# Kernel tuning notes

Measured on AMD Instinct MI355X. Metric: run time of the kernel, lower is better.

Reference implementation:

```python
import jax, jax.numpy as jnp
import numpy as np

B, N, H, D, F = 32, 128, 256, 256, 512   # batch, nodes, gru hidden, latent dim, mlp hidden
SUP = 0.5                                 # ancestor_suppression_strength
EPS = 1e-6


def _gru(x, h, Wx, Wh, bx, bh):
    """torch.nn.GRUCell math; x,h: [..., H]."""
    gx = x @ Wx + bx
    gh = h @ Wh + bh
    rx, ux, nx = jnp.split(gx, 3, axis=-1)
    rh, uh, nh = jnp.split(gh, 3, axis=-1)
    r = jax.nn.sigmoid(rx + rh)
    u = jax.nn.sigmoid(ux + uh)
    n = jnp.tanh(nx + r * nh)
    return (1.0 - u) * n + u * h


def setup_inputs() -> dict:
    key = jax.random.key(0)
    ks = jax.random.split(key, 12)
    rn = lambda k, shape, fan: jax.random.normal(k, shape, jnp.float32) * (fan ** -0.5)
    return {
        "z": jax.random.normal(ks[0], (B, D), jnp.float32),
        "targets": jax.random.randint(ks[1], (B, N, N), 0, 2, jnp.int32),
        "W_init": rn(ks[2], (D, H), D),
        "b_init": jnp.zeros((H,), jnp.float32),
        "Wx": rn(ks[3], (H, 3 * H), H),
        "Wh": rn(ks[4], (H, 3 * H), H),
        "bx": jnp.zeros((3 * H,), jnp.float32),
        "bh": jnp.zeros((3 * H,), jnp.float32),
        "W1": rn(ks[5], (2 * H + D, F), 2 * H + D),
        "b1": jnp.zeros((F,), jnp.float32),
        "W2": rn(ks[6], (F, 1), F),
        "b2": jnp.zeros((1,), jnp.float32),
    }


def reference(z, targets, W_init, b_init, Wx, Wh, bx, bh, W1, b1, W2, b2):
    # teacher-forcing link targets: strictly lower-triangular (parents have smaller index)
    tgt = jnp.tril(targets.astype(jnp.float32), k=-1)  # [B,N,N]
    idx = jnp.arange(N)

    def decode_one(z1, t1):  # z1:[D], t1:[N,N]
        h0 = jnp.tanh(z1 @ W_init + b_init)                      # decoder_init: z -> node-0 state
        states0 = jnp.zeros((N, H), jnp.float32).at[0].set(h0)
        A0 = jnp.zeros((N, N), jnp.float32)                      # ancestor bitset: A[i,j]=1 iff j ancestor of i

        def step(carry, t):
            states, A, ll = carry
            m = (idx < t).astype(jnp.float32)                    # existing-node mask
            pooled = (states * m[:, None]).sum(0) / m.sum()      # mean aggregation
            h_prov = _gru(pooled, h0, Wx, Wh, bx, bh)            # provisional new-node state
            # parent logits: MLP([h_new, h_j, z]) for every existing node j
            feat = jnp.concatenate([jnp.broadcast_to(h_prov, (N, H)), states,
                                    jnp.broadcast_to(z1, (N, D))], axis=-1)   # [N, 2H+D]
            logits = (jax.nn.relu(feat @ W1 + b1) @ W2 + b2)[:, 0]            # [N]
            row = t1[t]                                          # teacher-forced parents of node t
            anc = jnp.minimum(row @ A, 1.0)                      # j already ancestor of a chosen parent
            q = jnp.clip(jax.nn.sigmoid(logits) * (1.0 - SUP * anc), EPS, 1.0 - EPS)
            ll = ll + (m * (row * jnp.log(q) + (1.0 - row) * jnp.log1p(-q))).sum()
            A = A.at[t].set(jnp.minimum(row + row @ A, 1.0))     # ancestors(t) = parents U their ancestors
            states = states.at[t].set(h_prov)
            m2 = (idx <= t).astype(jnp.float32)[:, None]
            pooled2 = (states * m2).sum(0) / m2.sum()
            upd = _gru(jnp.broadcast_to(pooled2, (N, H)), states, Wx, Wh, bx, bh)
            states = m2 * upd + (1.0 - m2) * states              # propagate info among generated nodes
            return (states, A, ll), None

        (states, A, ll), _ = jax.lax.scan(step, (states0, A0, jnp.zeros((), jnp.float32)),
                                          jnp.arange(1, N))
        return t1, ll                                            # link matrix (teacher forced), log-likelihood

    L, ll = jax.vmap(decode_one)(z, tgt)
    return L, ll
```

## Files before the change

### kernel.cpp

```cpp
#include <hip/hip_runtime.h>
#include <hip/hip_bf16.h>
#include <math.h>

#define Bz 32
#define Nn 128
#define Hh 256
#define Dd 256
#define Ff 512
#define Gg 768
#define NT 512

typedef short v8s __attribute__((ext_vector_type(8)));
typedef float f4  __attribute__((ext_vector_type(4)));
#define MFMA(a,b,c) __builtin_amdgcn_mfma_f32_16x16x32_bf16(a,b,c,0,0,0)

#define WS_H0    0
#define WS_GH0   (WS_H0 + Bz*Hh)
#define WS_ZW1   (WS_GH0 + Bz*Gg)
#define WS_GXP   (WS_ZW1 + Bz*Ff)
#define WS_LOGP  (WS_GXP + Bz*2*8*Gg)
#define WS_BAR   (WS_LOGP + Bz*2*8*Nn)
#define WS_XS    (WS_BAR + Bz*32)
#define WS_WB    (WS_XS + Bz*32768)

#define SM_SW    0
#define SM_SST   81920
#define SM_NLDS  147456
#define SM_GXF   155648
#define SM_HPF   158720
#define SM_GX2   159232
#define SM_GHT   159616
#define SM_BASE  160000
#define SM_BHS   160256
#define SM_PSN   160640
#define SM_LOGI  160768
#define SM_TGR   161280
#define SM_RBIT  161536
#define SM_ANCW  161568
#define SM_AMASK 161600
#define SMEM_SZ  163648

__device__ __forceinline__ unsigned short f2bf(float x) {
  unsigned u = __float_as_uint(x);
  u = u + 0x7fffu + ((u >> 16) & 1u);
  return (unsigned short)(u >> 16);
}
__device__ __forceinline__ unsigned pack2(float e, float o) {
  return (unsigned)f2bf(e) | ((unsigned)f2bf(o) << 16);
}
__device__ __forceinline__ unsigned pkbf(float x, float y) {
  __hip_bfloat162 h = __float22bfloat162_rn(make_float2(x, y));
  union { __hip_bfloat162 h; unsigned u; } c; c.h = h; return c.u;
}
__device__ __forceinline__ float bf2f(unsigned short s) {
  return __uint_as_float(((unsigned)s) << 16);
}
__device__ __forceinline__ float sigm(float x) { return 1.0f / (1.0f + __expf(-x)); }
__device__ __forceinline__ float tanh_fast(float x) { return 2.0f / (1.0f + __expf(-2.0f*x)) - 1.0f; }
__device__ __forceinline__ v8s u4v(uint4 q) { union { uint4 q; v8s v; } c; c.q = q; return c.v; }

__device__ __forceinline__ void ast32(unsigned* p, unsigned v) {
  __hip_atomic_store(p, v, __ATOMIC_RELAXED, __HIP_MEMORY_SCOPE_AGENT);
}
__device__ __forceinline__ unsigned ald32(const unsigned* p) {
  return __hip_atomic_load(p, __ATOMIC_RELAXED, __HIP_MEMORY_SCOPE_AGENT);
}
__device__ __forceinline__ void ast64(unsigned long long* p, unsigned long long v) {
  __hip_atomic_store(p, v, __ATOMIC_RELAXED, __HIP_MEMORY_SCOPE_AGENT);
}
__device__ __forceinline__ unsigned long long ald64(const unsigned long long* p) {
  return __hip_atomic_load(p, __ATOMIC_RELAXED, __HIP_MEMORY_SCOPE_AGENT);
}

__device__ __forceinline__ void waitflags(const unsigned* FLG, int lane, int r, unsigned tgt)
{
  const bool watch = (lane < 8) && (lane != r);
  for (;;) {
    const unsigned f = watch ? ald32(FLG + lane) : 0xFFFFFFFFu;
    if (__ballot(f >= tgt) == 0xFFFFFFFFFFFFFFFFull) break;
  }
  __atomic_signal_fence(__ATOMIC_ACQUIRE);
}

__global__ void __launch_bounds__(256) prep_init(
    const int* __restrict__ tg, const float* __restrict__ Wx,
    const float* __restrict__ Wh, const float* __restrict__ W1,
    float* __restrict__ ws, float* __restrict__ out)
{
  const int stride = gridDim.x * blockDim.x;
  const int t0 = blockIdx.x * blockDim.x + threadIdx.x;

  for (int i = t0; i < Bz*Nn*Nn; i += stride) {
    int col = i & (Nn-1), row = (i >> 7) & (Nn-1);
    out[i] = (col < row) ? (float)tg[i] : 0.0f;
  }
  for (int i = t0; i < Bz; i += stride) out[Bz*Nn*Nn + i] = 0.0f;

  unsigned* BARu = (unsigned*)(ws + WS_BAR);
  for (int i = t0; i < Bz*32; i += stride) BARu[i] = 0u;

  unsigned* Wb = (unsigned*)(ws + WS_WB);
  for (int i = t0; i < 160*2048; i += stride) {
    int jw = i & 3, l = (i >> 2) & 63, ks = (i >> 8) & 7, nt = i >> 11;
    int k = ks*32 + (l >> 4)*8 + 2*jw;
    int n16 = l & 15;
    float lo, hi;
    if (nt < 48)       { int c = nt*16 + n16;        lo = Wh[k*Gg + c];      hi = Wh[(k+1)*Gg + c]; }
    else if (nt < 80)  { int f = (nt-48)*16 + n16;   lo = W1[(Hh+k)*Ff + f]; hi = W1[(Hh+k+1)*Ff + f]; }
    else if (nt < 128) { int c = (nt-80)*16 + n16;   lo = Wx[k*Gg + c];      hi = Wx[(k+1)*Gg + c]; }
    else               { int f = (nt-128)*16 + n16;  lo = W1[k*Ff + f];      hi = W1[(k+1)*Ff + f]; }
    Wb[i] = pack2(lo, hi);
  }
}

__global__ void __launch_bounds__(256) prep_batch(
    const float* __restrict__ z, const float* __restrict__ Wi,
    const float* __restrict__ bi, const float* __restrict__ Wh,
    const float* __restrict__ bh, const float* __restrict__ W1,
    float* __restrict__ ws)
{
  const int b = blockIdx.x, tid = threadIdx.x;
  __shared__ float zs[Dd], h0s[Hh];
  zs[tid] = z[b*Dd + tid];
  __syncthreads();
  float acc = bi[tid];
  for (int d = 0; d < Dd; ++d) acc = fmaf(zs[d], Wi[d*Hh + tid], acc);
  const float h0 = tanhf(acc);
  h0s[tid] = h0;
  ws[WS_H0 + b*Hh + tid] = h0;
  __syncthreads();
  for (int g = tid; g < Gg; g += 256) {
    float a = bh[g];
    for (int h = 0; h < Hh; ++h) a = fmaf(h0s[h], Wh[h*Gg + g], a);
    ws[WS_GH0 + b*Gg + g] = a;
  }
  for (int f = tid; f < Ff; f += 256) {
    float a = 0.0f;
    for (int d = 0; d < Dd; ++d) a = fmaf(zs[d], W1[(2*Hh + d)*Ff + f], a);
    ws[WS_ZW1 + b*Ff + f] = a;
  }
}

__device__ __forceinline__ void G_mfma(const unsigned short* SST, const uint4* SW4,
    int mt0, bool do1, int lane, f4* acc)
{
  #pragma unroll
  for (int ks = 0; ks < 8; ++ks) {
    const v8s a0 = *(const v8s*)(SST + (mt0*8 + ks)*512 + lane*8);
    const v8s w0 = u4v(SW4[(0*8 + ks)*64 + lane]);
    const v8s w1 = u4v(SW4[(1*8 + ks)*64 + lane]);
    const v8s w2 = u4v(SW4[(2*8 + ks)*64 + lane]);
    const v8s w3 = u4v(SW4[(3*8 + ks)*64 + lane]);
    const v8s w4 = u4v(SW4[(4*8 + ks)*64 + lane]);
    const v8s w5 = u4v(SW4[(5*8 + ks)*64 + lane]);
    acc[0] = MFMA(a0,w0,acc[0]); acc[1] = MFMA(a0,w1,acc[1]);
    acc[2] = MFMA(a0,w2,acc[2]); acc[3] = MFMA(a0,w3,acc[3]);
    acc[4] = MFMA(a0,w4,acc[4]); acc[5] = MFMA(a0,w5,acc[5]);
    if (do1) {
      const v8s a1 = *(const v8s*)(SST + ((mt0+1)*8 + ks)*512 + lane*8);
      acc[6]  = MFMA(a1,w0,acc[6]);  acc[7]  = MFMA(a1,w1,acc[7]);
      acc[8]  = MFMA(a1,w2,acc[8]);  acc[9]  = MFMA(a1,w3,acc[9]);
      acc[10] = MFMA(a1,w4,acc[10]); acc[11] = MFMA(a1,w5,acc[11]);
    }
  }
}

__device__ __forceinline__ void G_epi(const f4* ac, int mt, int t, int r,
    int quad, int c16, int lane, const float* GX2, const float* BHS,
    const unsigned short* SST, unsigned short* NLDS, float* PSN)
{
  #pragma unroll
  for (int ct = 0; ct < 2; ++ct) {
    const int hcl = ct*16 + c16;
    const f4 cr = ac[0 + ct], cu = ac[2 + ct], cn = ac[4 + ct];
    const float gxr = GX2[hcl], gxu = GX2[32+hcl], gxn = GX2[64+hcl];
    const float bhr = BHS[hcl], bhu = BHS[32+hcl], bhn = BHS[64+hcl];
    float colsum = 0.0f;
    #pragma unroll
    for (int rg = 0; rg < 4; ++rg) {
      const int row = mt*16 + quad*4 + rg;
      if (row < t) {
        const int spi = ((hcl>>3)*16 + quad*4 + rg)*8 + (hcl & 7);
        const float old = bf2f(SST[(mt*8 + r)*512 + spi]);
        const float rv = sigm(gxr + cr[rg] + bhr);
        const float uv = sigm(gxu + cu[rg] + bhu);
        const float nv = tanh_fast(gxn + rv*(cn[rg] + bhn));
        const float ns = (1.0f-uv)*nv + uv*old;
        NLDS[mt*512 + spi] = f2bf(ns);
        colsum += ns;
      }
    }
    colsum += __shfl_down(colsum, 16);
    colsum += __shfl_down(colsum, 32);
    if (lane < 16) atomicAdd(&PSN[ct*16 + lane], colsum);
  }
}

__device__ __forceinline__ void L_mfma(const unsigned short* SST, const uint4* SW4,
    int mt0, bool do1, int lane, f4* acc)
{
  #pragma unroll
  for (int ks = 0; ks < 8; ++ks) {
    const v8s a0 = *(const v8s*)(SST + (mt0*8 + ks)*512 + lane*8);
    const v8s c0 = u4v(SW4[(6*8 + ks)*64 + lane]);
    const v8s c1 = u4v(SW4[(7*8 + ks)*64 + lane]);
    const v8s c2 = u4v(SW4[(8*8 + ks)*64 + lane]);
    const v8s c3 = u4v(SW4[(9*8 + ks)*64 + lane]);
    acc[0] = MFMA(a0,c0,acc[0]); acc[1] = MFMA(a0,c1,acc[1]);
    acc[2] = MFMA(a0,c2,acc[2]); acc[3] = MFMA(a0,c3,acc[3]);
    if (do1) {
      const v8s a1 = *(const v8s*)(SST + ((mt0+1)*8 + ks)*512 + lane*8);
      acc[4] = MFMA(a1,c0,acc[4]); acc[5] = MFMA(a1,c1,acc[5]);
      acc[6] = MFMA(a1,c2,acc[6]); acc[7] = MFMA(a1,c3,acc[7]);
    }
  }
}

__device__ __forceinline__ void L_epi(const f4* ac, int mt, int t,
    int quad, int c16, const float* BASE, const float* w2r, float* LOGI)
{
  #pragma unroll
  for (int rg = 0; rg < 4; ++rg) {
    float v = fmaxf(ac[0][rg] + BASE[c16],    0.0f)*w2r[0]
            + fmaxf(ac[1][rg] + BASE[16+c16], 0.0f)*w2r[1]
            + fmaxf(ac[2][rg] + BASE[32+c16], 0.0f)*w2r[2]
            + fmaxf(ac[3][rg] + BASE[48+c16], 0.0f)*w2r[3];
    v += __shfl_xor(v, 1); v += __shfl_xor(v, 2);
    v += __shfl_xor(v, 4); v += __shfl_xor(v, 8);
    const int row = mt*16 + quad*4 + rg;
    if (c16 == 0 && row < t) atomicAdd(&LOGI[row], v);
  }
}

__device__ __forceinline__ void ll_gen(int tg_, int r, int lane, float b2v,
    const unsigned* LOGPb, const unsigned* RBIT, const unsigned* ANCW,
    float* out_ll)
{
  const int pp = tg_ & 1;
  const int row = 16*r + (lane >> 2);
  float term = 0.0f;
  if (row < tg_) {
    const unsigned* Lp = LOGPb + pp*1024;
    const int rr = (lane & 3)*2;
    float s = __uint_as_float(ald32(Lp + rr*128 + row))
            + __uint_as_float(ald32(Lp + (rr+1)*128 + row));
    s += __shfl_xor(s, 1); s += __shfl_xor(s, 2);
    if ((lane & 3) == 0) {
      const int w = row >> 5;
      const float anc = (float)((ANCW[pp*4 + w] >> (row & 31)) & 1u);
      float q = sigm(b2v + s) * (1.0f - 0.5f*anc);
      q = fminf(fmaxf(q, 1e-6f), 1.0f - 1e-6f);
      const unsigned rb = (RBIT[pp*4 + w] >> (row & 31)) & 1u;
      term = rb ? logf(q) : log1pf(-q);
    }
  }
  #pragma unroll
  for (int off = 1; off < 64; off <<= 1) term += __shfl_xor(term, off);
  if (lane == 0) atomicAdd(out_ll, term);
}

__global__ void __launch_bounds__(NT) decoder_main(
    const int* __restrict__ tg,
    const float* __restrict__ bx, const float* __restrict__ bh,
    const float* __restrict__ b1, const float* __restrict__ W2,
    const float* __restrict__ b2,
    float* __restrict__ ws, float* __restrict__ out)
{
  const int blk = blockIdx.x;
  const int b = blk & 31, r = blk >> 5;
  const int tid = threadIdx.x;
  const int lane = tid & 63, wv = tid >> 6;
  const int c16 = lane & 15, quad = lane >> 4;

  extern __shared__ char smem[];
  uint4* SW4 = (uint4*)(smem + SM_SW);
  unsigned short* SST = (unsigned short*)(smem + SM_SST);
  unsigned long long* SST64 = (unsigned long long*)(smem + SM_SST);
  unsigned short* NLDS = (unsigned short*)(smem + SM_NLDS);
  unsigned* NLDSu = (unsigned*)(smem + SM_NLDS);
  unsigned long long* NLDS64 = (unsigned long long*)(smem + SM_NLDS);
  float* GXF  = (float*)(smem + SM_GXF);
  unsigned short* HPF = (unsigned short*)(smem + SM_HPF);
  float* GX2  = (float*)(smem + SM_GX2);
  float* GHT  = (float*)(smem + SM_GHT);
  float* BASE = (float*)(smem + SM_BASE);
  float* BHS  = (float*)(smem + SM_BHS);
  float* PSN  = (float*)(smem + SM_PSN);
  float* LOGI = (float*)(smem + SM_LOGI);
  unsigned char* TGRu = (unsigned char*)(smem + SM_TGR);
  unsigned* RBIT  = (unsigned*)(smem + SM_RBIT);
  unsigned* ANCW  = (unsigned*)(smem + SM_ANCW);
  unsigned* AMASK = (unsigned*)(smem + SM_AMASK);

  const float* __restrict__ h0g  = ws + WS_H0  + b*Hh;
  const float* __restrict__ gh0g = ws + WS_GH0 + b*Gg;
  const float* __restrict__ zW1g = ws + WS_ZW1 + b*Ff;
  unsigned* GXPb = (unsigned*)(ws + WS_GXP) + b*2*8*Gg;
  unsigned* LOGPb = (unsigned*)(ws + WS_LOGP) + b*2*8*Nn;
  unsigned* FLG = (unsigned*)(ws + WS_BAR) + b*32;
  unsigned long long* XS64b = (unsigned long long*)(ws + WS_XS) + b*16384;
  const uint4* WB4 = (const uint4*)(ws + WS_WB);
  float* out_ll = out + Bz*Nn*Nn + b;

  for (int i = tid; i < 16384; i += NT) ((unsigned*)SST)[i] = 0u;
  for (int i = tid; i < 4096; i += NT) NLDSu[i] = 0u;
  for (int i = tid; i < 5120; i += NT) {
    const int lt = i >> 9, q = i & 511;
    int gt;
    if (lt < 6) { const int gate = lt >> 1, tt = lt & 1; gt = gate*16 + 2*r + tt; }
    else        { gt = 48 + 4*r + (lt - 6); }
    SW4[lt*512 + q] = WB4[gt*512 + q];
  }
  for (int i = tid; i < Nn*4; i += NT) AMASK[i] = 0u;
  if (tid < 96) BHS[tid] = bh[(tid >> 5)*256 + 32*r + (tid & 31)];
  if (tid < 128) TGRu[128 + tid] = (unsigned char)tg[b*Nn*Nn + 1*Nn + tid];
  float w2r[4];
  #pragma unroll
  for (int ft = 0; ft < 4; ++ft) w2r[ft] = W2[64*r + ft*16 + c16];
  const float b2v = b2[0];
  float p_bx[3][4], p_gh[3][4], p_h0[4];
  #pragma unroll
  for (int k = 0; k < 4; ++k) {
    const int c = 4*lane + k;
    p_h0[k] = h0g[c];
    #pragma unroll
    for (int g3 = 0; g3 < 3; ++g3) {
      p_bx[g3][k] = bx[g3*256 + c];
      p_gh[g3][k] = gh0g[g3*256 + c];
    }
  }
  int colj[2]; float auxj[2];
  #pragma unroll
  for (int jj = 0; jj < 2; ++jj) {
    const int j = 2*wv + jj;
    colj[jj] = 0; auxj[jj] = 0.0f;
    if (j >= 6 && j < 12) {
      const int jx = j - 6, g = jx >> 1, tt = jx & 1;
      const int col = g*256 + 32*r + tt*16 + c16;
      colj[jj] = col; auxj[jj] = bx[col];
    } else if (j >= 12) {
      const int ft = j - 12, f = 64*r + ft*16 + c16;
      auxj[jj] = zW1g[f] + b1[f];
    }
  }
  __syncthreads();
  if (tid < Hh) {
    const int c = tid;
    SST[(c>>5)*512 + ((c>>3)&3)*128 + (c&7)] = f2bf(h0g[c]);
  }
  if (tid < 32) PSN[tid] = h0g[32*r + tid];
  __syncthreads();
  {
    union { unsigned u[4]; v8s v; } cv;
    const float4 a0 = *(const float4*)(PSN + quad*8);
    const float4 a1 = *(const float4*)(PSN + quad*8 + 4);
    cv.u[0] = pkbf(a0.x, a0.y); cv.u[1] = pkbf(a0.z, a0.w);
    cv.u[2] = pkbf(a1.x, a1.y); cv.u[3] = pkbf(a1.z, a1.w);
    const v8s avp = cv.v;
    unsigned* GXPw = GXPb + 1*8*Gg + r*Gg;
    #pragma unroll
    for (int k2 = 0; k2 < 6; ++k2) {
      const int nt = wv*6 + k2;
      f4 c = {0.0f,0.0f,0.0f,0.0f};
      c = MFMA(avp, u4v(WB4[(80 + nt)*512 + r*64 + lane]), c);
      if (quad == 0) ast32(GXPw + nt*16 + c16, __float_as_uint(c[0]));
    }
  }
  if (tid < 128) ast64(XS64b + r*128 + tid, SST64[r*128 + tid]);
  __builtin_amdgcn_s_waitcnt(0x0F70);
  __syncthreads();
  if (tid == 0) { __atomic_signal_fence(__ATOMIC_RELEASE); ast32(FLG + r, 1u); }

  for (int t = 1; t < Nn; ++t) {
    const int tp = t & 1;
    const float invt  = 1.0f / (float)t;
    const float invt1 = 1.0f / (float)(t + 1);
    const int Mr   = (t + 15) >> 4;
    const int Mtot = (t + 16) >> 4;
    const int mtc  = t >> 4;
    const int nG = (Mr + 1) >> 1, nL = (Mr + 1) >> 1;
    const int njobs = nG + nL;

    waitflags(FLG, lane, r, (unsigned)t);

    if (tid < 384) {
      const unsigned long long* GXPr = (const unsigned long long*)(GXPb + tp*8*Gg);
      unsigned long long g[8];
      #pragma unroll
      for (int rr = 0; rr < 8; ++rr) g[rr] = ald64(GXPr + rr*384 + tid);
      float s0 = 0.0f, s1 = 0.0f;
      #pragma unroll
      for (int rr = 0; rr < 8; ++rr) {
        s0 += __uint_as_float((unsigned)g[rr]);
        s1 += __uint_as_float((unsigned)(g[rr] >> 32));
      }
      GXF[2*tid]   = s0;
      GXF[2*tid+1] = s1;
    }
    if (tid < 448) {
      const unsigned long long* XSr = XS64b + ((t-1)&1)*8192;
      for (int i = tid; i < Mr*1024; i += 448) {
        if (((i >> 7) & 7) != r) SST64[i] = ald64(XSr + i);
      }
    }
    if (wv == 6) {
      const int v0 = TGRu[tp*128 + lane];
      const int v1 = TGRu[tp*128 + lane + 64];
      const unsigned long long bal0 = __ballot(lane < t && v0);
      const unsigned long long bal1 = __ballot((lane + 64) < t && v1);
      if (lane == 0) {
        RBIT[tp*4+0] = (unsigned)bal0; RBIT[tp*4+1] = (unsigned)(bal0 >> 32);
        RBIT[tp*4+2] = (unsigned)bal1; RBIT[tp*4+3] = (unsigned)(bal1 >> 32);
      }
      LOGI[lane] = 0.0f; LOGI[lane+64] = 0.0f;
      if (lane < 32) PSN[lane] = 0.0f;
      unsigned m0=0,m1=0,m2=0,m3=0;
      if (lane < t && v0) {
        m0 = AMASK[lane*4+0]; m1 = AMASK[lane*4+1];
        m2 = AMASK[lane*4+2]; m3 = AMASK[lane*4+3];
      }
      if (lane + 64 < t && v1) {
        m0 |= AMASK[(lane+64)*4+0]; m1 |= AMASK[(lane+64)*4+1];
        m2 |= AMASK[(lane+64)*4+2]; m3 |= AMASK[(lane+64)*4+3];
      }
      #pragma unroll
      for (int off = 1; off < 64; off <<= 1) {
        m0 |= __shfl_xor(m0, off); m1 |= __shfl_xor(m1, off);
        m2 |= __shfl_xor(m2, off); m3 |= __shfl_xor(m3, off);
      }
      if (lane == 0) {
        ANCW[tp*4+0] = m0; ANCW[tp*4+1] = m1;
        ANCW[tp*4+2] = m2; ANCW[tp*4+3] = m3;
      }
    }
    if (wv == 7 && t > 1) ll_gen(t-1, r, lane, b2v, LOGPb, RBIT, ANCW, out_ll);
    __syncthreads();

    {
      float hp[4];
      const float* gr = GXF + 4*lane;
      #pragma unroll
      for (int k = 0; k < 4; ++k) {
        const float rv = sigm(gr[k]*invt       + p_bx[0][k] + p_gh[0][k]);
        const float uv = sigm(gr[256+k]*invt   + p_bx[1][k] + p_gh[1][k]);
        const float nv = tanh_fast(gr[512+k]*invt + p_bx[2][k] + rv*p_gh[2][k]);
        hp[k] = (1.0f - uv)*nv + uv*p_h0[k];
      }
      uint2 pk;
      pk.x = pack2(hp[0], hp[1]); pk.y = pack2(hp[2], hp[3]);
      *(uint2*)(HPF + 4*lane) = pk;
      if (wv == 0 && lane < 4)
        AMASK[t*4 + lane] = RBIT[tp*4 + lane] | ANCW[tp*4 + lane];
      if (wv == 1 && (t & 15) == 0) {
        for (int q = lane; q < 256; q += 64) NLDSu[mtc*256 + q] = 0u;
      }
      v8s av[8];
      #pragma unroll
      for (int ks = 0; ks < 8; ++ks) av[ks] = *(const v8s*)(HPF + ks*32 + quad*8);
      #pragma unroll
      for (int jj = 0; jj < 2; ++jj) {
        const int j = 2*wv + jj;
        f4 c = {0.0f,0.0f,0.0f,0.0f};
        if (j < 6) {
          #pragma unroll
          for (int ks = 0; ks < 8; ++ks) c = MFMA(av[ks], u4v(SW4[(j*8 + ks)*64 + lane]), c);
          if (quad == 0) GHT[(j>>1)*32 + (j&1)*16 + c16] = c[0];
        } else if (j < 12) {
          const int jx = j - 6, g = jx >> 1, tt = jx & 1;
          const uint4* Bp = WB4 + (80 + g*16 + 2*r + tt)*512 + lane;
          #pragma unroll
          for (int ks = 0; ks < 8; ++ks) c = MFMA(av[ks], u4v(Bp[ks*64]), c);
          if (quad == 0) GX2[g*32 + tt*16 + c16] = (c[0] + GXF[colj[jj]])*invt1 + auxj[jj];
        } else {
          const int ft = j - 12;
          const uint4* Bp = WB4 + (128 + 4*r + ft)*512 + lane;
          #pragma unroll
          for (int ks = 0; ks < 8; ++ks) c = MFMA(av[ks], u4v(Bp[ks*64]), c);
          if (quad == 0) BASE[ft*16 + c16] = c[0] + auxj[jj];
        }
      }
    }
    __syncthreads();

    if (wv < njobs) {
      if (wv < nG) {
        const int mt0 = 2*wv;
        const bool do1 = (mt0 + 1 < Mr);
        f4 acc[12];
        #pragma unroll
        for (int i = 0; i < 12; ++i) acc[i] = (f4){0.0f,0.0f,0.0f,0.0f};
        G_mfma(SST, SW4, mt0, do1, lane, acc);
        G_epi(acc, mt0, t, r, quad, c16, lane, GX2, BHS, SST, NLDS, PSN);
        if (do1) G_epi(acc+6, mt0+1, t, r, quad, c16, lane, GX2, BHS, SST, NLDS, PSN);
      } else {
        const int mt0 = 2*(wv - nG);
        const bool do1 = (mt0 + 1 < Mr);
        f4 acc[8];
        #pragma unroll
        for (int i = 0; i < 8; ++i) acc[i] = (f4){0.0f,0.0f,0.0f,0.0f};
        L_mfma(SST, SW4, mt0, do1, lane, acc);
        L_epi(acc, mt0, t, quad, c16, BASE, w2r, LOGI);
        if (do1) L_epi(acc+4, mt0+1, t, quad, c16, BASE, w2r, LOGI);
      }
    }
    if (wv == 7 && lane < 32) {
      const int hcl = lane;
      const float rv = sigm(GX2[hcl]    + GHT[hcl]    + BHS[hcl]);
      const float uv = sigm(GX2[32+hcl] + GHT[32+hcl] + BHS[32+hcl]);
      const float nv = tanh_fast(GX2[64+hcl] + rv*(GHT[64+hcl] + BHS[64+hcl]));
      const float old = bf2f(HPF[32*r + hcl]);
      const float ns = (1.0f - uv)*nv + uv*old;
      const int spi = ((hcl>>3)*16 + (t & 15))*8 + (hcl & 7);
      NLDS[mtc*512 + spi] = f2bf(ns);
      atomicAdd(&PSN[hcl], ns);
    }
    __syncthreads();

    {
      union { unsigned u[4]; v8s v; } cv;
      const float4 a0 = *(const float4*)(PSN + quad*8);
      const float4 a1 = *(const float4*)(PSN + quad*8 + 4);
      cv.u[0] = pkbf(a0.x, a0.y); cv.u[1] = pkbf(a0.z, a0.w);
      cv.u[2] = pkbf(a1.x, a1.y); cv.u[3] = pkbf(a1.z, a1.w);
      const v8s avp = cv.v;
      unsigned* GXPw = GXPb + ((t+1)&1)*8*Gg + r*Gg;
      #pragma unroll
      for (int k2 = 0; k2 < 6; ++k2) {
        const int nt = wv*6 + k2;
        f4 c = {0.0f,0.0f,0.0f,0.0f};
        c = MFMA(avp, u4v(WB4[(80 + nt)*512 + r*64 + lane]), c);
        if (quad == 0) ast32(GXPw + nt*16 + c16, __float_as_uint(c[0]));
      }
    }
    {
      unsigned long long* XSw = XS64b + tp*8192;
      for (int i = tid; i < Mtot*128; i += NT) {
        const int mt = i >> 7, q = i & 127;
        const unsigned long long v = NLDS64[i];
        ast64(XSw + (mt*8 + r)*128 + q, v);
        SST64[(mt*8 + r)*128 + q] = v;
      }
    }
    if (tid < 64)
      ast64((unsigned long long*)LOGPb + tp*512 + r*64 + tid,
            ((const unsigned long long*)LOGI)[tid]);
    if (wv == 7 && t + 1 < Nn) {
      const int base = b*Nn*Nn + (t+1)*Nn;
      TGRu[((t+1)&1)*128 + lane]      = (unsigned char)tg[base + lane];
      TGRu[((t+1)&1)*128 + lane + 64] = (unsigned char)tg[base + lane + 64];
    }
    __builtin_amdgcn_s_waitcnt(0x0F70);
    __syncthreads();
    if (tid == 0) { __atomic_signal_fence(__ATOMIC_RELEASE); ast32(FLG + r, (unsigned)(t + 1)); }
  }

  if (wv == 7) {
    waitflags(FLG, lane, r, (unsigned)Nn);
    ll_gen(Nn - 1, r, lane, b2v, LOGPb, RBIT, ANCW, out_ll);
  }
}

extern "C" void kernel_launch(void* const* d_in, const int* in_sizes, int n_in,
                              void* d_out, int out_size, void* d_ws, size_t ws_size,
                              hipStream_t stream)
{
  const float* z  = (const float*)d_in[0];
  const int*   tg = (const int*)  d_in[1];
  const float* Wi = (const float*)d_in[2];
  const float* bi = (const float*)d_in[3];
  const float* Wx = (const float*)d_in[4];
  const float* Wh = (const float*)d_in[5];
  const float* bx = (const float*)d_in[6];
  const float* bh = (const float*)d_in[7];
  const float* W1 = (const float*)d_in[8];
  const float* b1 = (const float*)d_in[9];
  const float* W2 = (const float*)d_in[10];
  const float* b2 = (const float*)d_in[11];
  float* out = (float*)d_out;
  float* ws  = (float*)d_ws;

  hipFuncSetAttribute((const void*)decoder_main,
                      hipFuncAttributeMaxDynamicSharedMemorySize, SMEM_SZ);

  hipLaunchKernelGGL(prep_init, dim3(512), dim3(256), 0, stream, tg, Wx, Wh, W1, ws, out);
  hipLaunchKernelGGL(prep_batch, dim3(Bz), dim3(256), 0, stream, z, Wi, bi, Wh, bh, W1, ws);

  void* args[] = { (void*)&tg, (void*)&bx, (void*)&bh, (void*)&b1,
                   (void*)&W2, (void*)&b2, (void*)&ws, (void*)&out };
  hipLaunchCooperativeKernel((void*)decoder_main, dim3(256), dim3(NT),
                             args, SMEM_SZ, stream);
}
```

Before: 2.341 ms.

## Double block to 1024 threads, overlap MFMA phases, use counter barrier across blocks

Result: slower. 3.254 ms (+39.0%).

```diff
diff --git a/kernel.cpp b/kernel.cpp
--- a/kernel.cpp
+++ b/kernel.cpp
@@ -8,7 +8,7 @@
 #define Dd 256
 #define Ff 512
 #define Gg 768
-#define NT 512
+#define NT 1024
 
 typedef short v8s __attribute__((ext_vector_type(8)));
 typedef float f4  __attribute__((ext_vector_type(4)));
@@ -72,14 +72,17 @@
   return __hip_atomic_load(p, __ATOMIC_RELAXED, __HIP_MEMORY_SCOPE_AGENT);
 }
 
-__device__ __forceinline__ void waitflags(const unsigned* FLG, int lane, int r, unsigned tgt)
-{
-  const bool watch = (lane < 8) && (lane != r);
-  for (;;) {
-    const unsigned f = watch ? ald32(FLG + lane) : 0xFFFFFFFFu;
-    if (__ballot(f >= tgt) == 0xFFFFFFFFFFFFFFFFull) break;
-  }
-  __atomic_signal_fence(__ATOMIC_ACQUIRE);
+__device__ __forceinline__ void bbar(unsigned* cnt, unsigned& seq)
+{
+  __builtin_amdgcn_s_waitcnt(0x0F70);
+  __syncthreads();
+  seq += 8;
+  if (threadIdx.x == 0) {
+    __hip_atomic_fetch_add(cnt, 1u, __ATOMIC_RELAXED, __HIP_MEMORY_SCOPE_AGENT);
+    while (__hip_atomic_load(cnt, __ATOMIC_RELAXED, __HIP_MEMORY_SCOPE_AGENT) < seq)
+      __builtin_amdgcn_s_sleep(1);
+  }
+  __syncthreads();
 }
 
 __global__ void __launch_bounds__(256) prep_init(
@@ -269,7 +272,7 @@
   const int blk = blockIdx.x;
   const int b = blk & 31, r = blk >> 5;
   const int tid = threadIdx.x;
-  const int lane = tid & 63, wv = tid >> 6;
+  const int lane = tid & 63, w = tid >> 6;
   const int c16 = lane & 15, quad = lane >> 4;
 
   extern __shared__ char smem[];
@@ -297,7 +300,7 @@
   const float* __restrict__ zW1g = ws + WS_ZW1 + b*Ff;
   unsigned* GXPb = (unsigned*)(ws + WS_GXP) + b*2*8*Gg;
   unsigned* LOGPb = (unsigned*)(ws + WS_LOGP) + b*2*8*Nn;
-  unsigned* FLG = (unsigned*)(ws + WS_BAR) + b*32;
+  unsigned* bar = (unsigned*)(ws + WS_BAR) + b*32;
   unsigned long long* XS64b = (unsigned long long*)(ws + WS_XS) + b*16384;
   const uint4* WB4 = (const uint4*)(ws + WS_WB);
   float* out_ll = out + Bz*Nn*Nn + b;
@@ -319,30 +322,33 @@
   for (int ft = 0; ft < 4; ++ft) w2r[ft] = W2[64*r + ft*16 + c16];
   const float b2v = b2[0];
   float p_bx[3][4], p_gh[3][4], p_h0[4];
-  #pragma unroll
-  for (int k = 0; k < 4; ++k) {
-    const int c = 4*lane + k;
-    p_h0[k] = h0g[c];
+  int colj[2]; float auxj[2];
+  if (w >= 8) {
     #pragma unroll
-    for (int g3 = 0; g3 < 3; ++g3) {
-      p_bx[g3][k] = bx[g3*256 + c];
-      p_gh[g3][k] = gh0g[g3*256 + c];
-    }
-  }
-  int colj[2]; float auxj[2];
-  #pragma unroll
-  for (int jj = 0; jj < 2; ++jj) {
-    const int j = 2*wv + jj;
-    colj[jj] = 0; auxj[jj] = 0.0f;
-    if (j >= 6 && j < 12) {
-      const int jx = j - 6, g = jx >> 1, tt = jx & 1;
-      const int col = g*256 + 32*r + tt*16 + c16;
-      colj[jj] = col; auxj[jj] = bx[col];
-    } else if (j >= 12) {
-      const int ft = j - 12, f = 64*r + ft*16 + c16;
-      auxj[jj] = zW1g[f] + b1[f];
-    }
-  }
+    for (int k = 0; k < 4; ++k) {
+      const int c = 4*lane + k;
+      p_h0[k] = h0g[c];
+      #pragma unroll
+      for (int g3 = 0; g3 < 3; ++g3) {
+        p_bx[g3][k] = bx[g3*256 + c];
+        p_gh[g3][k] = gh0g[g3*256 + c];
+      }
+    }
+    #pragma unroll
+    for (int jj = 0; jj < 2; ++jj) {
+      const int j = (w - 8) + 8*jj;
+      colj[jj] = 0; auxj[jj] = 0.0f;
+      if (j >= 6 && j < 12) {
+        const int jx = j - 6, g = jx >> 1, tt = jx & 1;
+        const int col = g*256 + 32*r + tt*16 + c16;
+        colj[jj] = col; auxj[jj] = bx[col];
+      } else if (j >= 12) {
+        const int ft = j - 12, f = 64*r + ft*16 + c16;
+        auxj[jj] = zW1g[f] + b1[f];
+      }
+    }
+  }
+  unsigned bseq = 0;
   __syncthreads();
   if (tid < Hh) {
     const int c = tid;
@@ -359,17 +365,15 @@
     const v8s avp = cv.v;
     unsigned* GXPw = GXPb + 1*8*Gg + r*Gg;
     #pragma unroll
-    for (int k2 = 0; k2 < 6; ++k2) {
-      const int nt = wv*6 + k2;
+    for (int k2 = 0; k2 < 3; ++k2) {
+      const int nt = w*3 + k2;
       f4 c = {0.0f,0.0f,0.0f,0.0f};
       c = MFMA(avp, u4v(WB4[(80 + nt)*512 + r*64 + lane]), c);
       if (quad == 0) ast32(GXPw + nt*16 + c16, __float_as_uint(c[0]));
     }
   }
   if (tid < 128) ast64(XS64b + r*128 + tid, SST64[r*128 + tid]);
-  __builtin_amdgcn_s_waitcnt(0x0F70);
-  __syncthreads();
-  if (tid == 0) { __atomic_signal_fence(__ATOMIC_RELEASE); ast32(FLG + r, 1u); }
+  bbar(bar, bseq);
 
   for (int t = 1; t < Nn; ++t) {
     const int tp = t & 1;
@@ -378,12 +382,12 @@
     const int Mr   = (t + 15) >> 4;
     const int Mtot = (t + 16) >> 4;
     const int mtc  = t >> 4;
-    const int nG = (Mr + 1) >> 1, nL = (Mr + 1) >> 1;
-    const int njobs = nG + nL;
-
-    waitflags(FLG, lane, r, (unsigned)t);
-
-    if (tid < 384) {
+    const int nG = (Mr + 1) >> 1;
+    const int njobs = 2*nG;
+    const unsigned long long* XSr = XS64b + (1-tp)*8192;
+    unsigned long long* XSw = XS64b + tp*8192;
+
+    if (w < 6) {
       const unsigned long long* GXPr = (const unsigned long long*)(GXPb + tp*8*Gg);
       unsigned long long g[8];
       #pragma unroll
@@ -396,24 +400,16 @@
       }
       GXF[2*tid]   = s0;
       GXF[2*tid+1] = s1;
-    }
-    if (tid < 448) {
-      const unsigned long long* XSr = XS64b + ((t-1)&1)*8192;
-      for (int i = tid; i < Mr*1024; i += 448) {
+    } else if (w < 14) {
+      const int idx = tid - 384;
+      for (int i = idx; i < Mr*1024; i += 512) {
         if (((i >> 7) & 7) != r) SST64[i] = ald64(XSr + i);
       }
-    }
-    if (wv == 6) {
+    } else if (w == 14) {
       const int v0 = TGRu[tp*128 + lane];
-      const int v1 = TGRu[tp*128 + lane + 64];
+      const int v1 = TGRu[tp*128 + 64 + lane];
       const unsigned long long bal0 = __ballot(lane < t && v0);
       const unsigned long long bal1 = __ballot((lane + 64) < t && v1);
-      if (lane == 0) {
-        RBIT[tp*4+0] = (unsigned)bal0; RBIT[tp*4+1] = (unsigned)(bal0 >> 32);
-        RBIT[tp*4+2] = (unsigned)bal1; RBIT[tp*4+3] = (unsigned)(bal1 >> 32);
-      }
-      LOGI[lane] = 0.0f; LOGI[lane+64] = 0.0f;
-      if (lane < 32) PSN[lane] = 0.0f;
       unsigned m0=0,m1=0,m2=0,m3=0;
       if (lane < t && v0) {
         m0 = AMASK[lane*4+0]; m1 = AMASK[lane*4+1];
@@ -428,82 +424,95 @@
         m0 |= __shfl_xor(m0, off); m1 |= __shfl_xor(m1, off);
         m2 |= __shfl_xor(m2, off); m3 |= __shfl_xor(m3, off);
       }
-      if (lane == 0) {
-        ANCW[tp*4+0] = m0; ANCW[tp*4+1] = m1;
-        ANCW[tp*4+2] = m2; ANCW[tp*4+3] = m3;
-      }
-    }
-    if (wv == 7 && t > 1) ll_gen(t-1, r, lane, b2v, LOGPb, RBIT, ANCW, out_ll);
+      LOGI[lane] = 0.0f; LOGI[lane + 64] = 0.0f;
+      if (lane < 32) PSN[lane] = 0.0f;
+      if (lane < 4) {
+        const unsigned rbw = (lane == 0) ? (unsigned)bal0 :
+                             (lane == 1) ? (unsigned)(bal0 >> 32) :
+                             (lane == 2) ? (unsigned)bal1 : (unsigned)(bal1 >> 32);
+        const unsigned anw = (lane == 0) ? m0 : (lane == 1) ? m1 : (lane == 2) ? m2 : m3;
+        RBIT[tp*4 + lane] = rbw;
+        ANCW[tp*4 + lane] = anw;
+      }
+    } else {
+      if (t > 1) ll_gen(t-1, r, lane, b2v, LOGPb, RBIT, ANCW, out_ll);
+    }
     __syncthreads();
 
-    {
-      float hp[4];
-      const float* gr = GXF + 4*lane;
-      #pragma unroll
-      for (int k = 0; k < 4; ++k) {
-        const float rv = sigm(gr[k]*invt       + p_bx[0][k] + p_gh[0][k]);
-        const float uv = sigm(gr[256+k]*invt   + p_bx[1][k] + p_gh[1][k]);
-        const float nv = tanh_fast(gr[512+k]*invt + p_bx[2][k] + rv*p_gh[2][k]);
-        hp[k] = (1.0f - uv)*nv + uv*p_h0[k];
-      }
-      uint2 pk;
-      pk.x = pack2(hp[0], hp[1]); pk.y = pack2(hp[2], hp[3]);
-      *(uint2*)(HPF + 4*lane) = pk;
-      if (wv == 0 && lane < 4)
+    f4 acc[12];
+    #pragma unroll
+    for (int i = 0; i < 12; ++i) acc[i] = (f4){0.0f,0.0f,0.0f,0.0f};
+    int kindA = 0, mtA = 0; bool haveA = false, d1A = false;
+    if (w < 8) {
+      if (w < njobs) {
+        haveA = true;
+        if (w < nG) { kindA = 0; mtA = 2*w; }
+        else        { kindA = 1; mtA = 2*(w - nG); }
+        d1A = (mtA + 1 < Mr);
+        if (kindA == 0) G_mfma(SST, SW4, mtA, d1A, lane, acc);
+        else            L_mfma(SST, SW4, mtA, d1A, lane, acc);
+      }
+    } else {
+      if (w == 8 && lane < 4)
         AMASK[t*4 + lane] = RBIT[tp*4 + lane] | ANCW[tp*4 + lane];
-      if (wv == 1 && (t & 15) == 0) {
+      if (w == 9 && (t & 15) == 0) {
         for (int q = lane; q < 256; q += 64) NLDSu[mtc*256 + q] = 0u;
       }
-      v8s av[8];
-      #pragma unroll
-      for (int ks = 0; ks < 8; ++ks) av[ks] = *(const v8s*)(HPF + ks*32 + quad*8);
-      #pragma unroll
-      for (int jj = 0; jj < 2; ++jj) {
-        const int j = 2*wv + jj;
-        f4 c = {0.0f,0.0f,0.0f,0.0f};
-        if (j < 6) {
-          #pragma unroll
-          for (int ks = 0; ks < 8; ++ks) c = MFMA(av[ks], u4v(SW4[(j*8 + ks)*64 + lane]), c);
-          if (quad == 0) GHT[(j>>1)*32 + (j&1)*16 + c16] = c[0];
-        } else if (j < 12) {
-          const int jx = j - 6, g = jx >> 1, tt = jx & 1;
-          const uint4* Bp = WB4 + (80 + g*16 + 2*r + tt)*512 + lane;
-          #pragma unroll
-          for (int ks = 0; ks < 8; ++ks) c = MFMA(av[ks], u4v(Bp[ks*64]), c);
-          if (quad == 0) GX2[g*32 + tt*16 + c16] = (c[0] + GXF[colj[jj]])*invt1 + auxj[jj];
+      {
+        float hp[4];
+        #pragma unroll
+        for (int k = 0; k < 4; ++k) {
+          const int c = 4*lane + k;
+          const float rv = sigm(GXF[c]*invt       + p_bx[0][k] + p_gh[0][k]);
+          const float uv = sigm(GXF[256+c]*invt   + p_bx[1][k] + p_gh[1][k]);
+          const float nv = tanh_fast(GXF[512+c]*invt + p_bx[2][k] + rv*p_gh[2][k]);
+          hp[k] = (1.0f - uv)*nv + uv*p_h0[k];
+        }
+        uint2 pk;
+        pk.x = pack2(hp[0], hp[1]); pk.y = pack2(hp[2], hp[3]);
+        *(uint2*)(HPF + 4*lane) = pk;
+      }
+      {
+        v8s av[8];
+        #pragma unroll
+        for (int ks = 0; ks < 8; ++ks) av[ks] = *(const v8s*)(HPF + ks*32 + quad*8);
+        #pragma unroll
+        for (int jj = 0; jj < 2; ++jj) {
+          const int j = (w - 8) + 8*jj;
+          f4 c = {0.0f,0.0f,0.0f,0.0f};
+          if (j < 6) {
+            #pragma unroll
+            for (int ks = 0; ks < 8; ++ks) c = MFMA(av[ks], u4v(SW4[(j*8 + ks)*64 + lane]), c);
+            if (quad == 0) GHT[(j>>1)*32 + (j&1)*16 + c16] = c[0];
+          } else if (j < 12) {
+            const int jx = j - 6, g = jx >> 1, tt = jx & 1;
+            const uint4* Bp = WB4 + (80 + g*16 + 2*r + tt)*512 + lane;
+            #pragma unroll
+            for (int ks = 0; ks < 8; ++ks) c = MFMA(av[ks], u4v(Bp[ks*64]), c);
+            if (quad == 0) GX2[g*32 + tt*16 + c16] = (c[0] + GXF[colj[jj]])*invt1 + auxj[jj];
+          } else {
+            const int ft = j - 12;
+            const uint4* Bp = WB4 + (128 + 4*r + ft)*512 + lane;
+            #pragma unroll
+            for (int ks = 0; ks < 8; ++ks) c = MFMA(av[ks], u4v(Bp[ks*64]), c);
+            if (quad == 0) BASE[ft*16 + c16] = c[0] + auxj[jj];
+          }
+        }
+      }
+    }
+    __syncthreads();
+
+    if (w < 8) {
+      if (haveA) {
+        if (kindA == 0) {
+          G_epi(acc,     mtA,   t, r, quad, c16, lane, GX2, BHS, SST, NLDS, PSN);
+          if (d1A) G_epi(acc+6, mtA+1, t, r, quad, c16, lane, GX2, BHS, SST, NLDS, PSN);
         } else {
-          const int ft = j - 12;
-          const uint4* Bp = WB4 + (128 + 4*r + ft)*512 + lane;
-          #pragma unroll
-          for (int ks = 0; ks < 8; ++ks) c = MFMA(av[ks], u4v(Bp[ks*64]), c);
-          if (quad == 0) BASE[ft*16 + c16] = c[0] + auxj[jj];
+          L_epi(acc,     mtA,   t, quad, c16, BASE, w2r, LOGI);
+          if (d1A) L_epi(acc+4, mtA+1, t, quad, c16, BASE, w2r, LOGI);
         }
       }
-    }
-    __syncthreads();
-
-    if (wv < njobs) {
-      if (wv < nG) {
-        const int mt0 = 2*wv;
-        const bool do1 = (mt0 + 1 < Mr);
-        f4 acc[12];
-        #pragma unroll
-        for (int i = 0; i < 12; ++i) acc[i] = (f4){0.0f,0.0f,0.0f,0.0f};
-        G_mfma(SST, SW4, mt0, do1, lane, acc);
-        G_epi(acc, mt0, t, r, quad, c16, lane, GX2, BHS, SST, NLDS, PSN);
-        if (do1) G_epi(acc+6, mt0+1, t, r, quad, c16, lane, GX2, BHS, SST, NLDS, PSN);
-      } else {
-        const int mt0 = 2*(wv - nG);
-        const bool do1 = (mt0 + 1 < Mr);
-        f4 acc[8];
-        #pragma unroll
-        for (int i = 0; i < 8; ++i) acc[i] = (f4){0.0f,0.0f,0.0f,0.0f};
-        L_mfma(SST, SW4, mt0, do1, lane, acc);
-        L_epi(acc, mt0, t, quad, c16, BASE, w2r, LOGI);
-        if (do1) L_epi(acc+4, mt0+1, t, quad, c16, BASE, w2r, LOGI);
-      }
-    }
-    if (wv == 7 && lane < 32) {
+    } else if (w == 8 && lane < 32) {
       const int hcl = lane;
       const float rv = sigm(GX2[hcl]    + GHT[hcl]    + BHS[hcl]);
       const float uv = sigm(GX2[32+hcl] + GHT[32+hcl] + BHS[32+hcl]);
@@ -525,39 +534,31 @@
       const v8s avp = cv.v;
       unsigned* GXPw = GXPb + ((t+1)&1)*8*Gg + r*Gg;
       #pragma unroll
-      for (int k2 = 0; k2 < 6; ++k2) {
-        const int nt = wv*6 + k2;
+      for (int k2 = 0; k2 < 3; ++k2) {
+        const int nt = w*3 + k2;
         f4 c = {0.0f,0.0f,0.0f,0.0f};
         c = MFMA(avp, u4v(WB4[(80 + nt)*512 + r*64 + lane]), c);
         if (quad == 0) ast32(GXPw + nt*16 + c16, __float_as_uint(c[0]));
       }
     }
-    {
-      unsigned long long* XSw = XS64b + tp*8192;
-      for (int i = tid; i < Mtot*128; i += NT) {
-        const int mt = i >> 7, q = i & 127;
-        const unsigned long long v = NLDS64[i];
-        ast64(XSw + (mt*8 + r)*128 + q, v);
-        SST64[(mt*8 + r)*128 + q] = v;
-      }
+    for (int i = tid; i < Mtot*128; i += NT) {
+      const int mt = i >> 7, q = i & 127;
+      const unsigned long long v = NLDS64[i];
+      ast64(XSw + (mt*8 + r)*128 + q, v);
+      SST64[(mt*8 + r)*128 + q] = v;
     }
     if (tid < 64)
       ast64((unsigned long long*)LOGPb + tp*512 + r*64 + tid,
             ((const unsigned long long*)LOGI)[tid]);
-    if (wv == 7 && t + 1 < Nn) {
+    if (w == 14 && t + 1 < Nn) {
       const int base = b*Nn*Nn + (t+1)*Nn;
       TGRu[((t+1)&1)*128 + lane]      = (unsigned char)tg[base + lane];
       TGRu[((t+1)&1)*128 + lane + 64] = (unsigned char)tg[base + lane + 64];
     }
-    __builtin_amdgcn_s_waitcnt(0x0F70);
-    __syncthreads();
-    if (tid == 0) { __atomic_signal_fence(__ATOMIC_RELEASE); ast32(FLG + r, (unsigned)(t + 1)); }
-  }
-
-  if (wv == 7) {
-    waitflags(FLG, lane, r, (unsigned)Nn);
-    ll_gen(Nn - 1, r, lane, b2v, LOGPb, RBIT, ANCW, out_ll);
-  }
+    bbar(bar, bseq);
+  }
+
+  if (w == 15) ll_gen(Nn - 1, r, lane, b2v, LOGPb, RBIT, ANCW, out_ll);
 }
 
 extern "C" void kernel_launch(void* const* d_in, const int* in_sizes, int n_in,
```
